# Kernel tuning notes

Hardware: AMD Instinct MI355X
Metric: run time of the kernel (lower is better)

Reference implementation:

```python
import jax, jax.numpy as jnp
import numpy as np

D_MODEL = 512; D_STATE = 32; D_HEAD = 64; G = 4; R = 2
D_INNER = 2 * D_MODEL            # expand=2 -> 1024
H = D_INNER // D_HEAD            # 16 heads
RATIO = H // G                   # 4 heads per group
CHUNK = 128; EPS = 1e-5
DIM_Z = D_INNER; DIM_X = D_INNER
DIM_B = G * D_STATE * R; DIM_C = DIM_B
D_PROJ = DIM_Z + DIM_X + DIM_B + DIM_C + G + G
BATCH = 1; SEQ = 2048


def setup_inputs() -> dict:
    key = jax.random.key(0)
    ks = jax.random.split(key, 10)
    u = jax.random.normal(ks[0], (BATCH, SEQ, D_MODEL), jnp.float32)
    W_in = jax.random.normal(ks[1], (D_MODEL, D_PROJ), jnp.float32) * 0.02
    b_in = jnp.zeros((D_PROJ,), jnp.float32)
    # dt bias init: inverse-softplus of log-uniform dt in [1e-3, 1e-1]
    dt0 = jnp.exp(jax.random.uniform(ks[2], (G,)) * (np.log(0.1) - np.log(0.001)) + np.log(0.001))
    inv_dt = dt0 + jnp.log(-jnp.expm1(-dt0))
    s = DIM_Z + DIM_X + DIM_B + DIM_C
    b_in = b_in.at[s:s + G].set(inv_dt).at[s + G:].set(-3.0)
    W_xup = jax.random.normal(ks[3], (D_HEAD, D_HEAD * R), jnp.float32) * (1.0 / np.sqrt(D_HEAD * R))
    W_ydown = jax.random.normal(ks[4], (D_HEAD * R, D_HEAD), jnp.float32) * (1.0 / np.sqrt(D_HEAD * R))
    A_log = jnp.log(jax.random.uniform(ks[5], (G,), minval=1.0, maxval=16.0))
    theta_log = jax.random.normal(ks[6], (G, D_STATE // 2), jnp.float32)
    D_param = jnp.ones((H,), jnp.float32)
    wB = jnp.ones((D_STATE * R,), jnp.float32)
    wC = jnp.ones((D_STATE * R,), jnp.float32)
    bias_B = jnp.ones((G, D_STATE, R), jnp.float32)
    bias_C = jnp.ones((G, D_STATE, R), jnp.float32)
    W_out = jax.random.normal(ks[7], (D_INNER, D_MODEL), jnp.float32) * 0.02
    return dict(u=u, W_in=W_in, b_in=b_in, W_xup=W_xup, W_ydown=W_ydown,
                A_log=A_log, theta_log=theta_log, D_param=D_param,
                wB=wB, wC=wC, bias_B=bias_B, bias_C=bias_C, W_out=W_out)


def rmsnorm(x, w):
    return x * jax.lax.rsqrt(jnp.mean(x * x, -1, keepdims=True) + EPS) * w


def apply_rope(x, angles):
    # x: (B,L,G,N,R)  angles: (B,L,G,N/2)  -- rotate (even, odd) pairs along N
    Bz, L, Gg, N, Rr = x.shape
    xr = x.reshape(Bz, L, Gg, N // 2, 2, Rr)
    re, im = xr[..., 0, :], xr[..., 1, :]
    c = jnp.cos(angles)[..., None]
    s = jnp.sin(angles)[..., None]
    out = jnp.stack([re * c - im * s, re * s + im * c], axis=-2)
    return out.reshape(Bz, L, Gg, N, Rr)


def segsum(x):
    # x: (..., T) log-decay -> (..., T, T) causal pairwise cumulative sums
    T = x.shape[-1]
    cs = jnp.cumsum(x, -1)
    seg = cs[..., :, None] - cs[..., None, :]
    mask = jnp.tril(jnp.ones((T, T), bool))
    return jnp.where(mask, seg, -jnp.inf)


def chunk_parallel_scan(u_in, dt, A, C):
    # u_in: (B,L,H,N,P)  dt: (B,L,H)  A: (H,)  C: (B,L,H,N,R)
    Bz, L, Hh, N, P = u_in.shape
    Rr = C.shape[-1]
    nc = L // CHUNK
    la = (dt * A).reshape(Bz, nc, CHUNK, Hh)                       # log alpha per chunk
    uc = u_in.reshape(Bz, nc, CHUNK, Hh, N, P)
    Cc = C.reshape(Bz, nc, CHUNK, Hh, N, Rr)
    Lm = jnp.exp(segsum(la.transpose(0, 1, 3, 2)))                 # (B,nc,H,cs,cs)
    h_intra = jnp.einsum('bchts,bcshnp->bcthnp', Lm, uc)           # intra-chunk states
    y_diag = jnp.einsum('bcthnp,bcthnr->bcthpr', h_intra, Cc)
    decay_chunk = jnp.exp(la.sum(2))                               # (B,nc,H)
    h_final = h_intra[:, :, -1]                                    # (B,nc,H,N,P)
    h0 = jnp.zeros((Bz, Hh, N, P), u_in.dtype)

    def step(h, inp):
        d, c = inp
        return h * d[..., None, None] + c, h

    h_last, h_states = jax.lax.scan(
        step, h0, (decay_chunk.transpose(1, 0, 2), h_final.transpose(1, 0, 2, 3, 4)))
    h_states = h_states.transpose(1, 0, 2, 3, 4)                   # state entering each chunk
    decay_intra = jnp.exp(jnp.cumsum(la, 2))                       # (B,nc,cs,H)
    C_scaled = Cc * decay_intra[..., None, None]
    y_off = jnp.einsum('bchnp,bcthnr->bcthpr', h_states, C_scaled)
    y = (y_diag + y_off).reshape(Bz, L, Hh, P, Rr)
    return y, h_last


def _forward(u, W_in, b_in, W_xup, W_ydown, A_log, theta_log, D_param, wB, wC, bias_B, bias_C, W_out):
    Bz, L, _ = u.shape
    N, P = D_STATE, D_HEAD
    proj = u @ W_in + b_in
    o = 0
    z = proj[..., o:o + DIM_Z]; o += DIM_Z
    x = proj[..., o:o + DIM_X]; o += DIM_X
    Bi = proj[..., o:o + DIM_B]; o += DIM_B
    Ci = proj[..., o:o + DIM_C]; o += DIM_C
    dt_raw = proj[..., o:o + G]; o += G
    lam_raw = proj[..., o:o + G]

    dt = jax.nn.softplus(dt_raw)                                   # (B,L,G)
    lam = jax.nn.sigmoid(lam_raw)                                  # trapezoidal coeff
    x = jax.nn.silu(x)

    Bm = rmsnorm(Bi.reshape(Bz, L, G, N * R), wB).reshape(Bz, L, G, N, R) + bias_B
    Cm = rmsnorm(Ci.reshape(Bz, L, G, N * R), wC).reshape(Bz, L, G, N, R) + bias_C

    # data-dependent RoPE: cumulative angles = cumsum_t(dt_t * theta)
    theta = jnp.exp(theta_log)                                     # (G, N/2)
    angles = jnp.cumsum(dt[..., None] * theta, axis=1)             # (B,L,G,N/2)
    Br = apply_rope(Bm, angles)
    Cr = apply_rope(Cm, angles)

    # expand group-shared dynamics to heads
    Bh = jnp.repeat(Br, RATIO, axis=2)                             # (B,L,H,N,R)
    Ch = jnp.repeat(Cr, RATIO, axis=2)
    dth = jnp.repeat(dt, RATIO, axis=2)                            # (B,L,H)
    lamh = jnp.repeat(lam, RATIO, axis=2)
    Ah = jnp.repeat(-jnp.exp(A_log), RATIO)                        # (H,)

    xh = x.reshape(Bz, L, H, P)
    x_up = (xh @ W_xup).reshape(Bz, L, H, P, R)                    # MIMO up-projection
    u_ssm = jnp.einsum('blhnr,blhpr->blhnp', Bh, x_up) * dth[..., None, None]
    # generalized trapezoidal rule: blend current and previous input contribution
    u_prev = jnp.pad(u_ssm[:, :-1], ((0, 0), (1, 0), (0, 0), (0, 0), (0, 0)))
    w = lamh[..., None, None]
    u_trap = w * u_ssm + (1.0 - w) * u_prev

    y, _h = chunk_parallel_scan(u_trap, dth, Ah, Ch)               # (B,L,H,P,R)
    y = y.reshape(Bz, L, H, P * R) @ W_ydown                       # MIMO down-projection
    y = y + D_param[None, None, :, None] * xh                      # skip connection
    y = y * jax.nn.silu(z.reshape(Bz, L, H, P))                    # gate
    return (y.reshape(Bz, L, D_INNER)) @ W_out


def reference(u, W_in, b_in, W_xup, W_ydown, A_log, theta_log, D_param, wB, wC, bias_B, bias_C, W_out):
    return _forward(u, W_in, b_in, W_xup, W_ydown, A_log, theta_log,
                    D_param, wB, wC, bias_B, bias_C, W_out)
```

## Files before the change

kernel.cpp:

```cpp
#include <hip/hip_runtime.h>
#include <hip/hip_bf16.h>

typedef __hip_bfloat16 bf16;
typedef __bf16 bfv8 __attribute__((ext_vector_type(8)));
typedef float fv4 __attribute__((ext_vector_type(4)));

__device__ __forceinline__ float bf2f(bf16 x){ return __bfloat162float(x); }
__device__ __forceinline__ bf16 f2bf(float x){ return __float2bfloat16(x); }
__device__ __forceinline__ float blo(unsigned u){ return __uint_as_float(u<<16); }
__device__ __forceinline__ float bhi(unsigned u){ return __uint_as_float(u & 0xffff0000u); }
struct __align__(8) bf4v { bf16 x,y,z,w; };
struct __align__(16) bf8s { ushort u[8]; };
__device__ __forceinline__ float4 ldb4(const bf16* p){
  ushort4 u = *(const ushort4*)p;
  float4 r;
  r.x = __uint_as_float(((unsigned)u.x)<<16);
  r.y = __uint_as_float(((unsigned)u.y)<<16);
  r.z = __uint_as_float(((unsigned)u.z)<<16);
  r.w = __uint_as_float(((unsigned)u.w)<<16);
  return r;
}
__device__ __forceinline__ void stb4(bf16* p, float4 v){
  bf4v t; t.x=f2bf(v.x); t.y=f2bf(v.y); t.z=f2bf(v.z); t.w=f2bf(v.w);
  *(bf4v*)p = t;
}

#define L_SEQ 2048
#define DPROJ 2568
#define NCHUNK 16
#define TCH 128

__device__ __forceinline__ void tbody(const float* __restrict__ in, bf16* __restrict__ out,
                                      int R, int C, int Cpad, int bx, int by, float (*t)[33])
{
  int c0 = bx*32, r0 = by*32;
  int tx = threadIdx.x & 31, ty = threadIdx.x >> 5;
  for (int i=0;i<32;i+=8){
    int r = r0+i+ty, cc = c0+tx;
    t[i+ty][tx] = (r<R && cc<C) ? in[(size_t)r*C+cc] : 0.f;
  }
  __syncthreads();
  for (int i=0;i<32;i+=8){
    int cc = c0+i+ty, r = r0+tx;
    if (cc<Cpad && r<R) out[(size_t)cc*R + r] = f2bf(t[tx][i+ty]);
  }
}

__global__ void prep(const float* __restrict__ Win, bf16* __restrict__ WinT,
                     const float* __restrict__ Wout, bf16* __restrict__ WoutT,
                     const float* __restrict__ Wyd, bf16* __restrict__ WydT,
                     const float* __restrict__ Wxup, bf16* __restrict__ WxupT)
{
  __shared__ float t[32][33];
  int b = blockIdx.x;
  if (b < 1344){
    tbody(Win, WinT, 512, DPROJ, 2688, b%84, b/84, t);
  } else if (b < 1856){
    int idx = b - 1344;
    tbody(Wout, WoutT, 1024, 512, 512, idx%16, idx/16, t);
  } else if (b < 1864){
    int idx = b - 1856;
    tbody(Wyd, WydT, 128, 64, 64, idx%2, idx/2, t);
  } else {
    int idx = b - 1864;
    tbody(Wxup, WxupT, 64, 128, 128, idx%4, idx/4, t);
  }
}

__global__ void __launch_bounds__(256) gemm1_mfma(const float* __restrict__ A, const bf16* __restrict__ BT,
                                                  const float* __restrict__ bias, bf16* __restrict__ C,
                                                  float* __restrict__ side)
{
  const int K = 512;
  __shared__ __align__(16) bf16 As[128*72];
  __shared__ __align__(16) bf16 Bs[128*72];
  int tid = threadIdx.x;
  int col0 = blockIdx.x*128, row0 = blockIdx.y*128;
  int wid = tid>>6, lane = tid&63;
  int wm = (wid&1)*64, wn = (wid>>1)*64;
  int lm = lane&15, lq = lane>>4;
  fv4 acc[4][4] = {};
  for (int k0=0;k0<K;k0+=64){
    #pragma unroll
    for (int i=0;i<4;i++){
      int e = tid + i*256;
      int r = e>>3, k8 = (e&7)*8;
      float4 a0 = *(const float4*)&A[(size_t)(row0+r)*K + k0 + k8];
      float4 a1 = *(const float4*)&A[(size_t)(row0+r)*K + k0 + k8 + 4];
      stb4(&As[r*72+k8],   a0);
      stb4(&As[r*72+k8+4], a1);
      *(bf8s*)&Bs[r*72+k8] = *(const bf8s*)&BT[(size_t)(col0+r)*K + k0 + k8];
    }
    __syncthreads();
    #pragma unroll
    for (int ks=0;ks<2;ks++){
      bfv8 af[4], bfr[4];
      #pragma unroll
      for (int mf=0;mf<4;mf++) af[mf] = *(const bfv8*)&As[(wm+mf*16+lm)*72 + ks*32 + lq*8];
      #pragma unroll
      for (int nf=0;nf<4;nf++) bfr[nf] = *(const bfv8*)&Bs[(wn+nf*16+lm)*72 + ks*32 + lq*8];
      #pragma unroll
      for (int mf=0;mf<4;mf++)
        #pragma unroll
        for (int nf=0;nf<4;nf++)
          acc[mf][nf] = __builtin_amdgcn_mfma_f32_16x16x32_bf16(af[mf], bfr[nf], acc[mf][nf], 0,0,0);
    }
    __syncthreads();
  }
  #pragma unroll
  for (int mf=0;mf<4;mf++){
    #pragma unroll
    for (int nf=0;nf<4;nf++){
      int gcol = col0 + wn + nf*16 + lm;
      if (gcol < DPROJ){
        float bia = bias[gcol];
        #pragma unroll
        for (int r=0;r<4;r++){
          int grow = row0 + wm + mf*16 + lq*4 + r;
          float v = acc[mf][nf][r] + bia;
          C[(size_t)grow*DPROJ + gcol] = f2bf(v);
          if (gcol >= 2560) side[grow*8 + (gcol-2560)] = v;
        }
      }
    }
  }
}

__global__ void __launch_bounds__(256) gemmo_mfma(const bf16* __restrict__ Yp, const bf16* __restrict__ BT,
                                                  float* __restrict__ C)
{
  const int K = 1024;
  __shared__ __align__(16) bf16 As[64*136];
  __shared__ __align__(16) bf16 Bs[64*136];
  int tid = threadIdx.x;
  int col0 = blockIdx.x*64, row0 = blockIdx.y*64;
  int wid = tid>>6, lane = tid&63;
  int wm = (wid&1)*32, wn = (wid>>1)*32;
  int lm = lane&15, lq = lane>>4;
  fv4 acc[2][2] = {};
  for (int k0=0;k0<K;k0+=128){
    #pragma unroll
    for (int i=0;i<4;i++){
      int e = tid + i*256;
      int m = e>>4, k8 = (e&15)*8;
      int kg = k0 + k8;
      *(bf8s*)&As[m*136+k8] = *(const bf8s*)&Yp[(size_t)(row0+m)*2048 + ((kg>>6)*128) + 64 + (kg&63)];
      *(bf8s*)&Bs[m*136+k8] = *(const bf8s*)&BT[(size_t)(col0+m)*K + kg];
    }
    __syncthreads();
    #pragma unroll
    for (int ks=0;ks<4;ks++){
      bfv8 af[2], bfr[2];
      #pragma unroll
      for (int mf=0;mf<2;mf++) af[mf] = *(const bfv8*)&As[(wm+mf*16+lm)*136 + ks*32 + lq*8];
      #pragma unroll
      for (int nf=0;nf<2;nf++) bfr[nf] = *(const bfv8*)&Bs[(wn+nf*16+lm)*136 + ks*32 + lq*8];
      #pragma unroll
      for (int mf=0;mf<2;mf++)
        #pragma unroll
        for (int nf=0;nf<2;nf++)
          acc[mf][nf] = __builtin_amdgcn_mfma_f32_16x16x32_bf16(af[mf], bfr[nf], acc[mf][nf], 0,0,0);
    }
    __syncthreads();
  }
  #pragma unroll
  for (int mf=0;mf<2;mf++)
    #pragma unroll
    for (int nf=0;nf<2;nf++){
      int gcol = col0 + wn + nf*16 + lm;
      #pragma unroll
      for (int r=0;r<4;r++){
        int grow = row0 + wm + mf*16 + lq*4 + r;
        C[(size_t)grow*512 + gcol] = acc[mf][nf][r];
      }
    }
}

__global__ void k23(const float* __restrict__ dlraw, float* __restrict__ dtb,
                    float* __restrict__ lamb, float* __restrict__ csdt)
{
  __shared__ float raw[L_SEQ*8];
  __shared__ float dts[L_SEQ*4];
  __shared__ float segs[4][64];
  int tid = threadIdx.x;
  for (int e=tid;e<L_SEQ*8;e+=256) raw[e] = dlraw[e];
  __syncthreads();
  int g = tid & 3, seg = tid >> 2;
  for (int i = 0; i < 32; i++){
    int l = seg*32 + i;
    float dr = raw[l*8 + g];
    float lr = raw[l*8 + 4 + g];
    float dt = (dr > 15.f) ? dr : log1pf(__expf(dr));
    dts[l*4+g] = dt;
    dtb[l*4+g] = dt;
    lamb[l*4+g] = 1.f/(1.f+__expf(-lr));
  }
  __syncthreads();
  float s = 0.f;
  for (int i=0;i<32;i++) s += dts[(seg*32+i)*4 + g];
  segs[g][seg] = s;
  __syncthreads();
  if (tid < 4) { float run = 0.f; for (int q=0;q<64;q++){ float t = segs[tid][q]; segs[tid][q] = run; run += t; } }
  __syncthreads();
  float run = segs[g][seg];
  for (int i=0;i<32;i++){ int l = seg*32+i; run += dts[l*4+g]; csdt[l*4+g] = run; }
}

__global__ void __launch_bounds__(256) k45x(
  const bf16* __restrict__ proj, const bf16* __restrict__ WxupT, bf16* __restrict__ xup,
  const float* __restrict__ wB, const float* __restrict__ wC,
  const float* __restrict__ biasB, const float* __restrict__ biasC,
  const float* __restrict__ theta_log, const float* __restrict__ csdt,
  bf16* __restrict__ Br, bf16* __restrict__ Cr)
{
  __shared__ __align__(16) bf16 As[128*72];
  __shared__ __align__(16) bf16 Bs[128*72];
  int tid = threadIdx.x;
  if (blockIdx.x < 256){
    int m0 = blockIdx.x*128;
    for (int e = tid; e < 1024; e += 256){
      int n = e>>3, k8 = (e&7)*8;
      *(bf8s*)&Bs[n*72 + k8] = *(const bf8s*)&WxupT[n*64 + k8];
    }
    for (int e = tid; e < 1024; e += 256){
      int r = e>>3, k8 = (e&7)*8;
      int m = m0 + r;
      int l = m >> 4, h = m & 15;
      bf8s v = *(const bf8s*)&proj[(size_t)l*DPROJ + 1024 + h*64 + k8];
      float s[8];
      #pragma unroll
      for (int j=0;j<8;j++){
        float x = blo((unsigned)v.u[j]);
        s[j] = x/(1.f+__expf(-x));
      }
      stb4(&As[r*72 + k8],     make_float4(s[0],s[1],s[2],s[3]));
      stb4(&As[r*72 + k8 + 4], make_float4(s[4],s[5],s[6],s[7]));
    }
    __syncthreads();
    int wid = tid>>6, lane = tid&63;
    int wm = (wid&1)*64, wn = (wid>>1)*64;
    int lm = lane&15, lq = lane>>4;
    fv4 acc[4][4] = {};
    #pragma unroll
    for (int kk=0;kk<64;kk+=32){
      bfv8 af[4], bfr[4];
      #pragma unroll
      for (int mf=0;mf<4;mf++) af[mf] = *(const bfv8*)&As[(wm+mf*16+lm)*72 + kk + lq*8];
      #pragma unroll
      for (int nf=0;nf<4;nf++) bfr[nf] = *(const bfv8*)&Bs[(wn+nf*16+lm)*72 + kk + lq*8];
      #pragma unroll
      for (int mf=0;mf<4;mf++)
        #pragma unroll
        for (int nf=0;nf<4;nf++)
          acc[mf][nf] = __builtin_amdgcn_mfma_f32_16x16x32_bf16(af[mf], bfr[nf], acc[mf][nf], 0,0,0);
    }
    #pragma unroll
    for (int mf=0;mf<4;mf++)
      #pragma unroll
      for (int nf=0;nf<4;nf++){
        int col = wn + nf*16 + lm;
        #pragma unroll
        for (int r=0;r<4;r++){
          int m = m0 + wm + mf*16 + lq*4 + r;
          xup[(size_t)m*128 + col] = f2bf(acc[mf][nf][r]);
        }
      }
  } else {
    int g = tid >> 6, idx = tid & 63;
    int k = idx >> 2;
    bool is_im = (idx >> 1) & 1;
    float th = __expf(theta_log[g*16+k]);
    float wBv = wB[idx], wCv = wC[idx];
    float bBv = biasB[g*64+idx], bCv = biasC[g*64+idx];
    #pragma unroll
    for (int i=0;i<8;i++){
      int l = (blockIdx.x-256)*8 + i;
      const bf16* pr = proj + (size_t)l*DPROJ;
      float bv = bf2f(pr[2048 + g*64 + idx]);
      float cv = bf2f(pr[2304 + g*64 + idx]);
      float sb = bv*bv, sc = cv*cv;
      #pragma unroll
      for (int off=32; off; off>>=1){ sb += __shfl_xor(sb, off); sc += __shfl_xor(sc, off); }
      float rb = rsqrtf(sb*(1.f/64.f) + 1e-5f);
      float rc = rsqrtf(sc*(1.f/64.f) + 1e-5f);
      float bm = bv*rb*wBv + bBv;
      float cm = cv*rc*wCv + bCv;
      float ang = csdt[l*4+g] * th;
      float ca = cosf(ang), sa = sinf(ang);
      float bp = __shfl_xor(bm, 2);
      float cp = __shfl_xor(cm, 2);
      float bo = is_im ? (bp*sa + bm*ca) : (bm*ca - bp*sa);
      float co = is_im ? (cp*sa + cm*ca) : (cm*ca - cp*sa);
      Br[((size_t)l*4+g)*64 + idx] = f2bf(bo);
      Cr[((size_t)l*4+g)*64 + idx] = f2bf(co);
    }
  }
}

__global__ void __launch_bounds__(256) k6y(
  const bf16* __restrict__ Br, const bf16* __restrict__ Cr, const bf16* __restrict__ xup,
  const float* __restrict__ dtb, const float* __restrict__ lamb, const float* __restrict__ A_log,
  bf16* __restrict__ ypr, bf16* __restrict__ hfin, float* __restrict__ dcb, float* __restrict__ csb)
{
  __shared__ __align__(16) bf16 Cs[64*40];
  __shared__ __align__(16) bf16 Bs[64*40];
  __shared__ __align__(16) bf16 Bsn[32*72];
  __shared__ __align__(16) bf16 Fs[64*72];
  __shared__ __align__(16) bf16 Xs[64*72];
  __shared__ float dt_l[128], lam_l[128], cs_l[128];
  __shared__ float u1s[160], u12s[160], vs_[32];
  int bx = blockIdx.x; int g = bx & 3, q = bx >> 2;
  int c = blockIdx.y;
  int h4 = blockIdx.z;
  int h = g*4 + h4;
  int tid = threadIdx.x;
  int l0 = c*TCH;
  int w = tid>>6, lane = tid&63, lm = lane&15, lq = lane>>4;
  float Ah = -__expf(A_log[g]);
  float dt_prev = (c>0) ? dtb[(l0-1)*4+g] : 0.f;
  if (tid<128){ dt_l[tid] = dtb[(l0+tid)*4+g]; lam_l[tid] = lamb[(l0+tid)*4+g]; }
  __syncthreads();
  if (tid < 64){
    float a = dt_l[2*tid]*Ah, b = dt_l[2*tid+1]*Ah;
    float s = a + b;
    #pragma unroll
    for (int off=1; off<64; off<<=1){
      float v = __shfl_up(s, off);
      if (tid >= off) s += v;
    }
    cs_l[2*tid+1] = s;
    cs_l[2*tid]   = s - b;
  }
  __syncthreads();
  float ref = cs_l[q*32+16];
  if (tid < 160){
    int jj = tid;
    float u1v = 0.f, u2v = 0.f;
    if (jj>=1 && jj<=128) u1v = lam_l[jj-1]*dt_l[jj-1]*__expf(fminf(ref-cs_l[jj-1],60.f));
    if (jj<=127){ float dtx = (jj>=1)? dt_l[jj-1] : dt_prev; u2v = (1.f-lam_l[jj])*dtx*__expf(fminf(ref-cs_l[jj],60.f)); }
    u1s[jj] = u1v; u12s[jj] = u1v+u2v;
  }
  if (tid < 32) vs_[tid] = __expf(fminf(cs_l[q*32+tid]-ref,60.f));
  for (int e4 = tid; e4 < 512; e4 += 256){
    int tl = e4>>4, c4 = (e4&15)*4;
    bf4v v = *(const bf4v*)&Cr[((size_t)(l0+q*32+tl)*4+g)*64 + c4];
    bf16 arr[4] = {v.x,v.y,v.z,v.w};
    #pragma unroll
    for (int i=0;i<4;i++){ int q6=c4+i; Cs[((tl<<1)|(q6&1))*40 + (q6>>1)] = arr[i]; }
  }
  __syncthreads();
  float vfin = __expf(fminf(cs_l[127]-ref,60.f));
  fv4 acc[4] = {};
  fv4 acch[2] = {};
  int nch = (q+2 < 5) ? (q+2) : 5;
  for (int kc=0; kc<nch; kc++){
    for (int e4 = tid; e4 < 512; e4 += 256){
      int jjloc = e4>>4, c4 = (e4&15)*4;
      int jj = kc*32 + jjloc; int l = l0-1+jj;
      bf4v v;
      if (l >= 0 && jj <= 128) v = *(const bf4v*)&Br[((size_t)l*4+g)*64 + c4];
      else { v.x=v.y=v.z=v.w = f2bf(0.f); }
      bf16 arr[4] = {v.x,v.y,v.z,v.w};
      #pragma unroll
      for (int i=0;i<4;i++){ int q6=c4+i; Bs[((q6&1)*32+jjloc)*40 + (q6>>1)] = arr[i]; }
      if (q == 3){
        float gcv = vfin * u12s[jj];
        #pragma unroll
        for (int i=0;i<4;i++){ int q6=c4+i; Bsn[(q6>>1)*72 + (q6&1)*32 + jjloc] = f2bf(gcv*bf2f(arr[i])); }
      }
    }
    for (int e4 = tid; e4 < 1024; e4 += 256){
      int jjloc = e4>>5, c4 = (e4&31)*4;
      int jj = kc*32+jjloc; int l = l0-1+jj;
      bf4v v;
      if (l>=0 && jj<=128) v = *(const bf4v*)&xup[((size_t)l*16 + h)*128 + c4];
      else { v.x=v.y=v.z=v.w = f2bf(0.f); }
      bf16 arr[4] = {v.x,v.y,v.z,v.w};
      #pragma unroll
      for (int i=0;i<4;i++){ int q7=c4+i; Xs[(q7>>1)*72 + (q7&1)*32 + jjloc] = arr[i]; }
    }
    __syncthreads();
    {
      bfv8 a = *(const bfv8*)&Cs[(w*16+lm)*40 + lq*8];
      fv4 zz = {0.f,0.f,0.f,0.f};
      int rb = w*16 + lq*4;
      float vA = vs_[rb>>1];
      float vB = vs_[(rb>>1)+1];
      #pragma unroll
      for (int nt=0;nt<4;nt++){
        bfv8 b = *(const bfv8*)&Bs[(nt*16+lm)*40 + lq*8];
        fv4 s = __builtin_amdgcn_mfma_f32_16x16x32_bf16(a, b, zz, 0,0,0);
        int col = nt*16+lm;
        int jj = kc*32 + (col&31);
        float u1v = u1s[jj], u12v = u12s[jj];
        #pragma unroll
        for (int r=0;r<4;r++){
          int row = rb + r;
          float vT = (r<2) ? vA : vB;
          float cf;
          if (kc < q) cf = u12v;
          else {
            int T = q*32 + (row>>1);
            if (kc == q) cf = (jj<=T) ? u12v : ((jj==T+1) ? u1v : 0.f);
            else         cf = (jj==T+1) ? u1v : 0.f;
          }
          Fs[row*72+col] = f2bf(cf*vT*s[r]);
        }
      }
    }
    __syncthreads();
    #pragma unroll
    for (int r2=0;r2<2;r2++){
      bfv8 a = *(const bfv8*)&Fs[(w*16+lm)*72 + r2*32 + lq*8];
      #pragma unroll
      for (int nt=0;nt<4;nt++){
        bfv8 b = *(const bfv8*)&Xs[(nt*16+lm)*72 + r2*32 + lq*8];
        acc[nt] = __builtin_amdgcn_mfma_f32_16x16x32_bf16(a, b, acc[nt], 0,0,0);
      }
    }
    if (q == 3){
      #pragma unroll
      for (int r2=0;r2<2;r2++){
        bfv8 a = *(const bfv8*)&Xs[(w*16+lm)*72 + r2*32 + lq*8];
        #pragma unroll
        for (int nt2=0;nt2<2;nt2++){
          bfv8 b = *(const bfv8*)&Bsn[(nt2*16+lm)*72 + r2*32 + lq*8];
          acch[nt2] = __builtin_amdgcn_mfma_f32_16x16x32_bf16(a, b, acch[nt2], 0,0,0);
        }
      }
    }
    __syncthreads();
  }
  #pragma unroll
  for (int nt=0;nt<4;nt++){
    int p = nt*16+lm;
    #pragma unroll
    for (int r=0;r<4;r++){
      int row = w*16+lq*4+r;
      int T = q*32+(row>>1), r1 = row&1;
      ypr[((size_t)(l0+T)*16 + h)*128 + p*2+r1] = f2bf(acc[nt][r]);
    }
  }
  if (q == 3){
    #pragma unroll
    for (int nt2=0;nt2<2;nt2++){
      int n = nt2*16+lm;
      #pragma unroll
      for (int r=0;r<4;r++){
        int p = w*16+lq*4+r;
        hfin[(((size_t)c*16+h)*64 + p)*32 + n] = f2bf(acch[nt2][r]);
      }
    }
    if (tid == 0) dcb[c*16+h] = __expf(cs_l[127]);
  }
  if (q == 0 && h4 == 0 && tid < 128) csb[(c*4+g)*128 + tid] = cs_l[tid];
}

__global__ void __launch_bounds__(256) k8af(
  const bf16* __restrict__ Cr, const bf16* __restrict__ hfin,
  const float* __restrict__ dcb, const float* __restrict__ csb,
  bf16* __restrict__ ypr, const bf16* __restrict__ WydT,
  const bf16* __restrict__ proj, const float* __restrict__ Dp)
{
  __shared__ __align__(16) char arena[52224];
  bf16* C2s = (bf16*)arena;
  bf16* hT  = (bf16*)(arena + 20480);
  float* cse = (float*)(arena + 25600);
  bf16* Yf  = (bf16*)arena;
  bf16* Wds = (bf16*)(arena + 34816);
  int h = blockIdx.x, c = blockIdx.y;
  int g = h >> 2;
  int tid = threadIdx.x;
  int l0 = c*TCH;
  int w = tid>>6, lane = tid&63, lm = lane&15, lq = lane>>4;
  for (int e4 = tid; e4 < 2048; e4 += 256){
    int tl = e4>>4, c4 = (e4&15)*4;
    bf4v v = *(const bf4v*)&Cr[((size_t)(l0+tl)*4+g)*64 + c4];
    bf16 arr[4] = {v.x,v.y,v.z,v.w};
    #pragma unroll
    for (int i=0;i<4;i++){ int q6=c4+i; C2s[((tl<<1)|(q6&1))*40 + (q6>>1)] = arr[i]; }
  }
  for (int e = tid; e < 1024; e += 256){
    int qq = e>>4, k8 = (e&15)*8;
    *(bf8s*)&Wds[qq*136 + k8] = *(const bf8s*)&WydT[qq*128 + k8];
  }
  {
    int e0 = tid*8;
    float carry[8] = {};
    for (int j = 0; j < c; j++){
      float dc = dcb[j*16+h];
      float4 a = ldb4(&hfin[((size_t)j*16+h)*2048 + e0]);
      float4 b = ldb4(&hfin[((size_t)j*16+h)*2048 + e0 + 4]);
      carry[0]=carry[0]*dc+a.x; carry[1]=carry[1]*dc+a.y; carry[2]=carry[2]*dc+a.z; carry[3]=carry[3]*dc+a.w;
      carry[4]=carry[4]*dc+b.x; carry[5]=carry[5]*dc+b.y; carry[6]=carry[6]*dc+b.z; carry[7]=carry[7]*dc+b.w;
    }
    int p = e0>>5, n = e0&31;
    stb4(&hT[p*40+n],   make_float4(carry[0],carry[1],carry[2],carry[3]));
    stb4(&hT[p*40+n+4], make_float4(carry[4],carry[5],carry[6],carry[7]));
  }
  if (tid < 128) cse[tid] = __expf(csb[(c*4+g)*128 + tid]);
  __syncthreads();
  float yfull[4][4][4];
  fv4 zz = {0.f,0.f,0.f,0.f};
  #pragma unroll
  for (int mi=0;mi<4;mi++){
    int mt = w*4 + mi;
    bfv8 a = *(const bfv8*)&C2s[(mt*16+lm)*40 + lq*8];
    #pragma unroll
    for (int nt=0;nt<4;nt++){
      bfv8 b = *(const bfv8*)&hT[(nt*16+lm)*40 + lq*8];
      fv4 s = __builtin_amdgcn_mfma_f32_16x16x32_bf16(a, b, zz, 0,0,0);
      int p = nt*16+lm;
      #pragma unroll
      for (int r=0;r<4;r++){
        int row = mt*16+lq*4+r;
        int tl = row>>1, r1 = row&1;
        float yd = bf2f(ypr[((size_t)(l0+tl)*16 + h)*128 + p*2 + r1]);
        yfull[mi][nt][r] = yd + cse[tl]*s[r];
      }
    }
  }
  __syncthreads();
  #pragma unroll
  for (int mi=0;mi<4;mi++){
    int mt = w*4 + mi;
    #pragma unroll
    for (int nt=0;nt<4;nt++){
      int p = nt*16+lm;
      #pragma unroll
      for (int r=0;r<4;r++){
        int row = mt*16+lq*4+r;
        int tl = row>>1, r1 = row&1;
        Yf[tl*136 + p*2 + r1] = f2bf(yfull[mi][nt][r]);
      }
    }
  }
  __syncthreads();
  fv4 acc2[2][4] = {};
  #pragma unroll
  for (int kq=0;kq<4;kq++){
    #pragma unroll
    for (int m2=0;m2<2;m2++){
      bfv8 a = *(const bfv8*)&Yf[((w*2+m2)*16+lm)*136 + kq*32 + lq*8];
      #pragma unroll
      for (int nt2=0;nt2<4;nt2++){
        bfv8 b = *(const bfv8*)&Wds[(nt2*16+lm)*136 + kq*32 + lq*8];
        acc2[m2][nt2] = __builtin_amdgcn_mfma_f32_16x16x32_bf16(a, b, acc2[m2][nt2], 0,0,0);
      }
    }
  }
  float dv = Dp[h];
  #pragma unroll
  for (int m2=0;m2<2;m2++){
    #pragma unroll
    for (int nt2=0;nt2<4;nt2++){
      int qq = nt2*16+lm;
      #pragma unroll
      for (int r=0;r<4;r++){
        int tl = (w*2+m2)*16 + lq*4 + r;
        size_t lrow = (size_t)(l0+tl)*DPROJ;
        float x = bf2f(proj[lrow + 1024 + h*64 + qq]);
        float z = bf2f(proj[lrow + h*64 + qq]);
        float xs = x/(1.f+__expf(-x));
        float zs = z/(1.f+__expf(-z));
        float outv = (acc2[m2][nt2][r] + dv*xs)*zs;
        ypr[((size_t)(l0+tl)*16 + h)*128 + 64 + qq] = f2bf(outv);
      }
    }
  }
}

extern "C" void kernel_launch(void* const* d_in, const int* in_sizes, int n_in,
                              void* d_out, int out_size, void* d_ws, size_t ws_size,
                              hipStream_t stream) {
  const float* u       = (const float*)d_in[0];
  const float* W_in    = (const float*)d_in[1];
  const float* b_in    = (const float*)d_in[2];
  const float* W_xup   = (const float*)d_in[3];
  const float* W_ydown = (const float*)d_in[4];
  const float* A_log   = (const float*)d_in[5];
  const float* theta_l = (const float*)d_in[6];
  const float* D_p     = (const float*)d_in[7];
  const float* wB      = (const float*)d_in[8];
  const float* wC      = (const float*)d_in[9];
  const float* biasB   = (const float*)d_in[10];
  const float* biasC   = (const float*)d_in[11];
  const float* W_out   = (const float*)d_in[12];
  float* out = (float*)d_out;

  char* w = (char*)d_ws;
  bf16*  proj  = (bf16*)(w);
  float* dlraw = (float*)(w + 10518528);
  float* dtb   = (float*)(w + 10584064);
  float* lamb  = (float*)(w + 10616832);
  float* csdt  = (float*)(w + 10649600);
  bf16*  Brb   = (bf16*)(w + 10682368);
  bf16*  Crb   = (bf16*)(w + 11730944);
  bf16*  xupb  = (bf16*)(w + 12779520);
  bf16*  hfin  = (bf16*)(w + 21168128);
  bf16*  WxupT = (bf16*)(w + 22216704);
  float* dcb   = (float*)(w + 23265280);
  float* csb   = (float*)(w + 23266304);
  bf16*  ypr   = (bf16*)(w + 23299072);
  bf16*  WinT  = (bf16*)(w + 23299072);
  bf16*  WoutT = (bf16*)(w + 33784832);
  bf16*  WydT  = (bf16*)(w + 34833408);

  prep<<<1872,256,0,stream>>>(W_in, WinT, W_out, WoutT, W_ydown, WydT, W_xup, WxupT);
  gemm1_mfma<<<dim3(21,16),256,0,stream>>>(u, WinT, b_in, proj, dlraw);
  k23<<<1,256,0,stream>>>(dlraw, dtb, lamb, csdt);
  k45x<<<512,256,0,stream>>>(proj, WxupT, xupb, wB, wC, biasB, biasC, theta_l, csdt, Brb, Crb);
  k6y<<<dim3(16,16,4),256,0,stream>>>(Brb, Crb, xupb, dtb, lamb, A_log, ypr, hfin, dcb, csb);
  k8af<<<dim3(16,16),256,0,stream>>>(Crb, hfin, dcb, csb, ypr, WydT, proj, D_p);
  gemmo_mfma<<<dim3(8,32),256,0,stream>>>(ypr, WoutT, out);
}
```

Baseline: 191.2 us.

## Merge four query sub-blocks of chunk scan into one 512-thread block sharing B/X loads

The intra-chunk scan kernel previously ran one 256-thread block per 32-row query sub-block, so each of the four blocks reloaded the same B and x_up tiles from global memory. The new kernel uses one 512-thread block per (group, chunk, head), with wave pairs handling each query sub-block. B and x_up tiles are now loaded once and shared, the C fragments are held in registers, and the per-row decay factor is applied at the output instead of inside the F tile. In exchange there are 4x fewer blocks (256), much more shared memory per block, and uneven work across waves because causal masking makes early sub-blocks idle for later key chunks.

```diff
diff --git a/kernel.cpp b/kernel.cpp
--- a/kernel.cpp
+++ b/kernel.cpp
@@ -297,25 +297,28 @@
   }
 }
 
-__global__ void __launch_bounds__(256) k6y(
+__global__ void __launch_bounds__(512) k6q(
   const bf16* __restrict__ Br, const bf16* __restrict__ Cr, const bf16* __restrict__ xup,
   const float* __restrict__ dtb, const float* __restrict__ lamb, const float* __restrict__ A_log,
   bf16* __restrict__ ypr, bf16* __restrict__ hfin, float* __restrict__ dcb, float* __restrict__ csb)
 {
-  __shared__ __align__(16) bf16 Cs[64*40];
-  __shared__ __align__(16) bf16 Bs[64*40];
-  __shared__ __align__(16) bf16 Bsn[32*72];
-  __shared__ __align__(16) bf16 Fs[64*72];
-  __shared__ __align__(16) bf16 Xs[64*72];
-  __shared__ float dt_l[128], lam_l[128], cs_l[128];
-  __shared__ float u1s[160], u12s[160], vs_[32];
-  int bx = blockIdx.x; int g = bx & 3, q = bx >> 2;
-  int c = blockIdx.y;
-  int h4 = blockIdx.z;
+  __shared__ __align__(16) char arena[63488];
+  bf16* CsB  = (bf16*)arena;
+  bf16* Fs4  = (bf16*)(arena + 5120);
+  bf16* Bs   = (bf16*)(arena + 41984);
+  bf16* Xs   = (bf16*)(arena + 47104);
+  float* dt_l = (float*)(arena + 56320);
+  float* lam_l= (float*)(arena + 56832);
+  float* cs_l = (float*)(arena + 57344);
+  float* u1s  = (float*)(arena + 57856);
+  float* u12s = (float*)(arena + 60416);
+  float* vs_  = (float*)(arena + 62976);
+  int g = blockIdx.x, c = blockIdx.y, h4 = blockIdx.z;
   int h = g*4 + h4;
   int tid = threadIdx.x;
   int l0 = c*TCH;
   int w = tid>>6, lane = tid&63, lm = lane&15, lq = lane>>4;
+  int qw = w>>1, rh = w&1;
   float Ah = -__expf(A_log[g]);
   float dt_prev = (c>0) ? dtb[(l0-1)*4+g] : 0.f;
   if (tid<128){ dt_l[tid] = dtb[(l0+tid)*4+g]; lam_l[tid] = lamb[(l0+tid)*4+g]; }
@@ -332,29 +335,39 @@
     cs_l[2*tid]   = s - b;
   }
   __syncthreads();
-  float ref = cs_l[q*32+16];
-  if (tid < 160){
-    int jj = tid;
+  for (int e = tid; e < 640; e += 512){
+    int qq = e/160, jj = e - qq*160;
+    float refq = cs_l[qq*32+16];
     float u1v = 0.f, u2v = 0.f;
-    if (jj>=1 && jj<=128) u1v = lam_l[jj-1]*dt_l[jj-1]*__expf(fminf(ref-cs_l[jj-1],60.f));
-    if (jj<=127){ float dtx = (jj>=1)? dt_l[jj-1] : dt_prev; u2v = (1.f-lam_l[jj])*dtx*__expf(fminf(ref-cs_l[jj],60.f)); }
-    u1s[jj] = u1v; u12s[jj] = u1v+u2v;
-  }
-  if (tid < 32) vs_[tid] = __expf(fminf(cs_l[q*32+tid]-ref,60.f));
-  for (int e4 = tid; e4 < 512; e4 += 256){
-    int tl = e4>>4, c4 = (e4&15)*4;
-    bf4v v = *(const bf4v*)&Cr[((size_t)(l0+q*32+tl)*4+g)*64 + c4];
-    bf16 arr[4] = {v.x,v.y,v.z,v.w};
-    #pragma unroll
-    for (int i=0;i<4;i++){ int q6=c4+i; Cs[((tl<<1)|(q6&1))*40 + (q6>>1)] = arr[i]; }
-  }
-  __syncthreads();
-  float vfin = __expf(fminf(cs_l[127]-ref,60.f));
-  fv4 acc[4] = {};
-  fv4 acch[2] = {};
-  int nch = (q+2 < 5) ? (q+2) : 5;
-  for (int kc=0; kc<nch; kc++){
-    for (int e4 = tid; e4 < 512; e4 += 256){
+    if (jj>=1 && jj<=128) u1v = lam_l[jj-1]*dt_l[jj-1]*__expf(fminf(refq-cs_l[jj-1],60.f));
+    if (jj<=127){ float dtx = (jj>=1)? dt_l[jj-1] : dt_prev; u2v = (1.f-lam_l[jj])*dtx*__expf(fminf(refq-cs_l[jj],60.f)); }
+    u1s[qq*160+jj] = u1v; u12s[qq*160+jj] = u1v+u2v;
+  }
+  if (tid < 128){ int qq = tid>>5, i = tid&31; vs_[tid] = __expf(fminf(cs_l[qq*32+i]-cs_l[qq*32+16],60.f)); }
+  bfv8 ca[2];
+  for (int qq=0; qq<4; qq++){
+    __syncthreads();
+    {
+      int e4 = tid;
+      int tl = e4>>4, c4 = (e4&15)*4;
+      bf4v v = *(const bf4v*)&Cr[((size_t)(l0+qq*32+tl)*4+g)*64 + c4];
+      bf16 arr[4] = {v.x,v.y,v.z,v.w};
+      #pragma unroll
+      for (int i=0;i<4;i++){ int q6=c4+i; CsB[((tl<<1)|(q6&1))*40 + (q6>>1)] = arr[i]; }
+    }
+    __syncthreads();
+    if (qw == qq){
+      ca[0] = *(const bfv8*)&CsB[(rh*32 +      lm)*40 + lq*8];
+      ca[1] = *(const bfv8*)&CsB[(rh*32 + 16 + lm)*40 + lq*8];
+    }
+  }
+  __syncthreads();
+  float vfin = __expf(fminf(cs_l[127]-cs_l[112],60.f));
+  fv4 acc[2][4] = {};
+  fv4 acch[2][2] = {};
+  for (int kc=0; kc<5; kc++){
+    {
+      int e4 = tid;
       int jjloc = e4>>4, c4 = (e4&15)*4;
       int jj = kc*32 + jjloc; int l = l0-1+jj;
       bf4v v;
@@ -363,13 +376,11 @@
       bf16 arr[4] = {v.x,v.y,v.z,v.w};
       #pragma unroll
       for (int i=0;i<4;i++){ int q6=c4+i; Bs[((q6&1)*32+jjloc)*40 + (q6>>1)] = arr[i]; }
-      if (q == 3){
-        float gcv = vfin * u12s[jj];
-        #pragma unroll
-        for (int i=0;i<4;i++){ int q6=c4+i; Bsn[(q6>>1)*72 + (q6&1)*32 + jjloc] = f2bf(gcv*bf2f(arr[i])); }
-      }
-    }
-    for (int e4 = tid; e4 < 1024; e4 += 256){
+      float gcv = vfin * u12s[480+jj];
+      #pragma unroll
+      for (int i=0;i<4;i++){ int q6=c4+i; CsB[(q6>>1)*72 + (q6&1)*32 + jjloc] = f2bf(gcv*bf2f(arr[i])); }
+    }
+    for (int e4 = tid; e4 < 1024; e4 += 512){
       int jjloc = e4>>5, c4 = (e4&31)*4;
       int jj = kc*32+jjloc; int l = l0-1+jj;
       bf4v v;
@@ -380,80 +391,92 @@
       for (int i=0;i<4;i++){ int q7=c4+i; Xs[(q7>>1)*72 + (q7&1)*32 + jjloc] = arr[i]; }
     }
     __syncthreads();
-    {
-      bfv8 a = *(const bfv8*)&Cs[(w*16+lm)*40 + lq*8];
+    if (kc < qw+2){
+      bf16* Fq = Fs4 + qw*4608;
       fv4 zz = {0.f,0.f,0.f,0.f};
-      int rb = w*16 + lq*4;
-      float vA = vs_[rb>>1];
-      float vB = vs_[(rb>>1)+1];
-      #pragma unroll
-      for (int nt=0;nt<4;nt++){
-        bfv8 b = *(const bfv8*)&Bs[(nt*16+lm)*40 + lq*8];
-        fv4 s = __builtin_amdgcn_mfma_f32_16x16x32_bf16(a, b, zz, 0,0,0);
-        int col = nt*16+lm;
-        int jj = kc*32 + (col&31);
-        float u1v = u1s[jj], u12v = u12s[jj];
+      #pragma unroll
+      for (int mt=0;mt<2;mt++){
+        int rb = rh*32 + mt*16 + lq*4;
+        #pragma unroll
+        for (int nt=0;nt<4;nt++){
+          bfv8 b = *(const bfv8*)&Bs[(nt*16+lm)*40 + lq*8];
+          fv4 s = __builtin_amdgcn_mfma_f32_16x16x32_bf16(ca[mt], b, zz, 0,0,0);
+          int col = nt*16+lm;
+          int jj = kc*32 + (col&31);
+          float u1v = u1s[qw*160+jj], u12v = u12s[qw*160+jj];
+          #pragma unroll
+          for (int r=0;r<4;r++){
+            int row = rb + r;
+            float cf;
+            if (kc < qw) cf = u12v;
+            else {
+              int T = qw*32 + (row>>1);
+              if (kc == qw) cf = (jj<=T) ? u12v : ((jj==T+1) ? u1v : 0.f);
+              else          cf = (jj==T+1) ? u1v : 0.f;
+            }
+            Fq[row*72+col] = f2bf(cf*s[r]);
+          }
+        }
+      }
+    }
+    __syncthreads();
+    if (kc < qw+2){
+      bf16* Fq = Fs4 + qw*4608;
+      #pragma unroll
+      for (int mt=0;mt<2;mt++)
+        #pragma unroll
+        for (int r2=0;r2<2;r2++){
+          bfv8 a = *(const bfv8*)&Fq[(rh*32+mt*16+lm)*72 + r2*32 + lq*8];
+          #pragma unroll
+          for (int nt=0;nt<4;nt++){
+            bfv8 b = *(const bfv8*)&Xs[(nt*16+lm)*72 + r2*32 + lq*8];
+            acc[mt][nt] = __builtin_amdgcn_mfma_f32_16x16x32_bf16(a, b, acc[mt][nt], 0,0,0);
+          }
+        }
+    }
+    if (qw == 3){
+      #pragma unroll
+      for (int mt=0;mt<2;mt++)
+        #pragma unroll
+        for (int r2=0;r2<2;r2++){
+          bfv8 a = *(const bfv8*)&Xs[(rh*32+mt*16+lm)*72 + r2*32 + lq*8];
+          #pragma unroll
+          for (int nt2=0;nt2<2;nt2++){
+            bfv8 b = *(const bfv8*)&CsB[(nt2*16+lm)*72 + r2*32 + lq*8];
+            acch[mt][nt2] = __builtin_amdgcn_mfma_f32_16x16x32_bf16(a, b, acch[mt][nt2], 0,0,0);
+          }
+        }
+    }
+    __syncthreads();
+  }
+  #pragma unroll
+  for (int mt=0;mt<2;mt++)
+    #pragma unroll
+    for (int nt=0;nt<4;nt++){
+      int p = nt*16+lm;
+      #pragma unroll
+      for (int r=0;r<4;r++){
+        int row = rh*32 + mt*16 + lq*4 + r;
+        int T = qw*32 + (row>>1), r1 = row&1;
+        float vT = vs_[qw*32 + (row>>1)];
+        ypr[((size_t)(l0+T)*16 + h)*128 + p*2+r1] = f2bf(acc[mt][nt][r]*vT);
+      }
+    }
+  if (qw == 3){
+    #pragma unroll
+    for (int mt=0;mt<2;mt++)
+      #pragma unroll
+      for (int nt2=0;nt2<2;nt2++){
+        int n = nt2*16+lm;
         #pragma unroll
         for (int r=0;r<4;r++){
-          int row = rb + r;
-          float vT = (r<2) ? vA : vB;
-          float cf;
-          if (kc < q) cf = u12v;
-          else {
-            int T = q*32 + (row>>1);
-            if (kc == q) cf = (jj<=T) ? u12v : ((jj==T+1) ? u1v : 0.f);
-            else         cf = (jj==T+1) ? u1v : 0.f;
-          }
-          Fs[row*72+col] = f2bf(cf*vT*s[r]);
+          int p = rh*32 + mt*16 + lq*4 + r;
+          hfin[(((size_t)c*16+h)*64 + p)*32 + n] = f2bf(acch[mt][nt2][r]);
         }
       }
-    }
-    __syncthreads();
-    #pragma unroll
-    for (int r2=0;r2<2;r2++){
-      bfv8 a = *(const bfv8*)&Fs[(w*16+lm)*72 + r2*32 + lq*8];
-      #pragma unroll
-      for (int nt=0;nt<4;nt++){
-        bfv8 b = *(const bfv8*)&Xs[(nt*16+lm)*72 + r2*32 + lq*8];
-        acc[nt] = __builtin_amdgcn_mfma_f32_16x16x32_bf16(a, b, acc[nt], 0,0,0);
-      }
-    }
-    if (q == 3){
-      #pragma unroll
-      for (int r2=0;r2<2;r2++){
-        bfv8 a = *(const bfv8*)&Xs[(w*16+lm)*72 + r2*32 + lq*8];
-        #pragma unroll
-        for (int nt2=0;nt2<2;nt2++){
-          bfv8 b = *(const bfv8*)&Bsn[(nt2*16+lm)*72 + r2*32 + lq*8];
-          acch[nt2] = __builtin_amdgcn_mfma_f32_16x16x32_bf16(a, b, acch[nt2], 0,0,0);
-        }
-      }
-    }
-    __syncthreads();
-  }
-  #pragma unroll
-  for (int nt=0;nt<4;nt++){
-    int p = nt*16+lm;
-    #pragma unroll
-    for (int r=0;r<4;r++){
-      int row = w*16+lq*4+r;
-      int T = q*32+(row>>1), r1 = row&1;
-      ypr[((size_t)(l0+T)*16 + h)*128 + p*2+r1] = f2bf(acc[nt][r]);
-    }
-  }
-  if (q == 3){
-    #pragma unroll
-    for (int nt2=0;nt2<2;nt2++){
-      int n = nt2*16+lm;
-      #pragma unroll
-      for (int r=0;r<4;r++){
-        int p = w*16+lq*4+r;
-        hfin[(((size_t)c*16+h)*64 + p)*32 + n] = f2bf(acch[nt2][r]);
-      }
-    }
-    if (tid == 0) dcb[c*16+h] = __expf(cs_l[127]);
-  }
-  if (q == 0 && h4 == 0 && tid < 128) csb[(c*4+g)*128 + tid] = cs_l[tid];
+  }
+  if (tid == 0) dcb[c*16+h] = __expf(cs_l[127]);
+  if (h4 == 0 && tid < 128) csb[(c*4+g)*128 + tid] = cs_l[tid];
 }
 
 __global__ void __launch_bounds__(256) k8af(
@@ -610,7 +633,7 @@
   gemm1_mfma<<<dim3(21,16),256,0,stream>>>(u, WinT, b_in, proj, dlraw);
   k23<<<1,256,0,stream>>>(dlraw, dtb, lamb, csdt);
   k45x<<<512,256,0,stream>>>(proj, WxupT, xupb, wB, wC, biasB, biasC, theta_l, csdt, Brb, Crb);
-  k6y<<<dim3(16,16,4),256,0,stream>>>(Brb, Crb, xupb, dtb, lamb, A_log, ypr, hfin, dcb, csb);
+  k6q<<<dim3(4,16,4),512,0,stream>>>(Brb, Crb, xupb, dtb, lamb, A_log, ypr, hfin, dcb, csb);
   k8af<<<dim3(16,16),256,0,stream>>>(Crb, hfin, dcb, csb, ypr, WydT, proj, D_p);
   gemmo_mfma<<<dim3(8,32),256,0,stream>>>(ypr, WoutT, out);
 }
```

New measurement: 306.4 us. 60.2% more time.
